# Kernel optimization log

Hardware: AMD Instinct MI355X
Metric: run time of the kernel (lower is better)

Reference implementation:

```python
import jax, jax.numpy as jnp
import numpy as np

LAMBDA = 1.5
B, N = 32, 2048


def setup_inputs() -> dict:
    key = jax.random.key(0)
    ks = jax.random.split(key, 8)
    return {
        "Y_r": jax.random.normal(ks[0], (B, N, N), jnp.float32),
        "Y_i": jax.random.normal(ks[1], (B, N, N), jnp.float32),
        "x_r": jax.random.normal(ks[2], (B, N, 1), jnp.float32),
        "x_i": jax.random.normal(ks[3], (B, N, 1), jnp.float32),
        "x_prev_r": jax.random.normal(ks[4], (B, N, 1), jnp.float32),
        "x_prev_i": jax.random.normal(ks[5], (B, N, 1), jnp.float32),
        "d3_w": jnp.ones((1, 1), jnp.float32),          # Dense(1), ones init
        "d3_b": jnp.zeros((1,), jnp.float32),
        "w1": jax.random.normal(ks[6], (1, 256), jnp.float32) * 0.1,
        "b1": jnp.zeros((256,), jnp.float32),
        "w2": jax.random.normal(ks[7], (256, 1), jnp.float32) * 0.1,
        "b2": jnp.zeros((1,), jnp.float32),
    }


def reference(Y_r, Y_i, x_r, x_i, x_prev_r, x_prev_i, d3_w, d3_b, w1, b1, w2, b2):
    L = LAMBDA
    # complex batched matvec: (B,N,N) @ (B,N,1) -> (B,N,1)
    x1_r = L * (jnp.matmul(Y_r, x_r) - jnp.matmul(Y_i, x_i))
    x1_i = L * (jnp.matmul(Y_r, x_i) + jnp.matmul(Y_i, x_r))
    # Dense(1) on trailing dim of size 1
    x1_r = x1_r @ d3_w + d3_b
    x1_i = x1_i @ d3_w + d3_b
    # |x|^2, mean over N (axis=1), keepdims -> (B,1,1)
    x_abs2_mean = jnp.mean(x_r ** 2 + x_i ** 2, axis=1, keepdims=True)
    scale = -(L ** 2) * (1.0 - x_abs2_mean)
    x1_r = x1_r + scale * x_prev_r
    x1_i = x1_i + scale * x_prev_i
    x1_abs = jnp.sqrt(x1_r ** 2 + x1_i ** 2)
    denom = jnp.maximum(x1_abs, 1e-12)
    # tiny MLP: Dense(256)+relu -> Dense(1) -> tanh
    h = jax.nn.relu(x1_abs @ w1 + b1)
    g = jnp.tanh(h @ w2 + b2)
    q = g / denom
    return (x1_r * q, x1_i * q)
```

## Files before the change

kernel.cpp:

```cpp
#include <hip/hip_runtime.h>
#include <math.h>

#define B_ 32
#define N_ 2048
#define ROWS_PER_BLOCK 16
#define BLOCKS_PER_BATCH (N_ / ROWS_PER_BLOCK)

__global__ __launch_bounds__(256) void scale_kernel(const float* __restrict__ x_r,
                                                    const float* __restrict__ x_i,
                                                    float* __restrict__ scale) {
    const int b = blockIdx.x;
    const int t = threadIdx.x;
    const float* xr = x_r + (size_t)b * N_;
    const float* xi = x_i + (size_t)b * N_;
    float s = 0.f;
    for (int i = t; i < N_; i += 256) {
        float a = xr[i], c = xi[i];
        s += a * a + c * c;
    }
    #pragma unroll
    for (int m = 1; m < 64; m <<= 1) s += __shfl_xor(s, m, 64);
    __shared__ float parts[4];
    if ((t & 63) == 0) parts[t >> 6] = s;
    __syncthreads();
    if (t == 0) {
        float tot = parts[0] + parts[1] + parts[2] + parts[3];
        scale[b] = -2.25f * (1.0f - tot / (float)N_);
    }
}

__global__ __launch_bounds__(256) void sync_block_kernel(
    const float* __restrict__ Yr, const float* __restrict__ Yi,
    const float* __restrict__ x_r, const float* __restrict__ x_i,
    const float* __restrict__ xp_r, const float* __restrict__ xp_i,
    const float* __restrict__ d3w, const float* __restrict__ d3b,
    const float* __restrict__ w1, const float* __restrict__ b1,
    const float* __restrict__ w2, const float* __restrict__ b2,
    const float* __restrict__ scale, float* __restrict__ out)
{
    __shared__ float4 xs_r[N_ / 4];
    __shared__ float4 xs_i[N_ / 4];

    const int t    = threadIdx.x;
    const int lane = t & 63;
    const int wave = t >> 6;
    const int b    = blockIdx.x / BLOCKS_PER_BATCH;
    const int row0 = (blockIdx.x % BLOCKS_PER_BATCH) * ROWS_PER_BLOCK;

    const float4* gxr = (const float4*)(x_r + (size_t)b * N_);
    const float4* gxi = (const float4*)(x_i + (size_t)b * N_);
    for (int i = t; i < N_ / 4; i += 256) {
        xs_r[i] = gxr[i];
        xs_i[i] = gxi[i];
    }
    __syncthreads();

    float w1v[4], b1v[4], w2v[4];
    #pragma unroll
    for (int k = 0; k < 4; ++k) {
        w1v[k] = w1[lane + 64 * k];
        b1v[k] = b1[lane + 64 * k];
        w2v[k] = w2[lane + 64 * k];
    }
    const float d3w_v = d3w[0], d3b_v = d3b[0], b2v = b2[0];
    const float sc = scale[b];

    #pragma unroll
    for (int r = 0; r < 4; ++r) {
        const int row = row0 + wave * 4 + r;
        const float4* yr4 = (const float4*)(Yr + ((size_t)b * N_ + row) * (size_t)N_);
        const float4* yi4 = (const float4*)(Yi + ((size_t)b * N_ + row) * (size_t)N_);

        float rr = 0.f, ri = 0.f, ir = 0.f, ii = 0.f;
        #pragma unroll
        for (int it = 0; it < 8; ++it) {
            const int idx = lane + it * 64;
            float4 a = yr4[idx];
            float4 c = yi4[idx];
            float4 u = xs_r[idx];
            float4 v = xs_i[idx];
            rr += a.x * u.x + a.y * u.y + a.z * u.z + a.w * u.w;
            ri += a.x * v.x + a.y * v.y + a.z * v.z + a.w * v.w;
            ir += c.x * u.x + c.y * u.y + c.z * u.z + c.w * u.w;
            ii += c.x * v.x + c.y * v.y + c.z * v.z + c.w * v.w;
        }
        #pragma unroll
        for (int m = 1; m < 64; m <<= 1) {
            rr += __shfl_xor(rr, m, 64);
            ri += __shfl_xor(ri, m, 64);
            ir += __shfl_xor(ir, m, 64);
            ii += __shfl_xor(ii, m, 64);
        }

        float x1r = 1.5f * (rr - ii);
        float x1i = 1.5f * (ri + ir);
        x1r = x1r * d3w_v + d3b_v;
        x1i = x1i * d3w_v + d3b_v;
        x1r += sc * xp_r[(size_t)b * N_ + row];
        x1i += sc * xp_i[(size_t)b * N_ + row];

        const float xabs  = sqrtf(x1r * x1r + x1i * x1i);
        const float denom = fmaxf(xabs, 1e-12f);

        float p = 0.f;
        #pragma unroll
        for (int k = 0; k < 4; ++k) {
            float h = fmaxf(xabs * w1v[k] + b1v[k], 0.f);
            p += h * w2v[k];
        }
        #pragma unroll
        for (int m = 1; m < 64; m <<= 1) p += __shfl_xor(p, m, 64);

        const float g = tanhf(p + b2v);
        const float q = g / denom;

        if (lane == 0) {
            out[(size_t)b * N_ + row]                    = x1r * q;
            out[(size_t)B_ * N_ + (size_t)b * N_ + row]  = x1i * q;
        }
    }
}

extern "C" void kernel_launch(void* const* d_in, const int* in_sizes, int n_in,
                              void* d_out, int out_size, void* d_ws, size_t ws_size,
                              hipStream_t stream) {
    const float* Yr   = (const float*)d_in[0];
    const float* Yi   = (const float*)d_in[1];
    const float* x_r  = (const float*)d_in[2];
    const float* x_i  = (const float*)d_in[3];
    const float* xp_r = (const float*)d_in[4];
    const float* xp_i = (const float*)d_in[5];
    const float* d3w  = (const float*)d_in[6];
    const float* d3b  = (const float*)d_in[7];
    const float* w1   = (const float*)d_in[8];
    const float* b1   = (const float*)d_in[9];
    const float* w2   = (const float*)d_in[10];
    const float* b2   = (const float*)d_in[11];
    float* out   = (float*)d_out;
    float* scale = (float*)d_ws;

    scale_kernel<<<B_, 256, 0, stream>>>(x_r, x_i, scale);
    sync_block_kernel<<<(B_ * N_) / ROWS_PER_BLOCK, 256, 0, stream>>>(
        Yr, Yi, x_r, x_i, xp_r, xp_i, d3w, d3b, w1, b1, w2, b2, scale, out);
}
```

Measured before the change: 977.1 us.

## Fuse scale reduction into matvec kernel and keep x in registers

```diff
diff --git a/kernel.cpp b/kernel.cpp
--- a/kernel.cpp
+++ b/kernel.cpp
@@ -3,57 +3,35 @@
 
 #define B_ 32
 #define N_ 2048
-#define ROWS_PER_BLOCK 16
+#define ROWS_PER_WAVE 4
+#define WAVES_PER_BLOCK 4
+#define ROWS_PER_BLOCK (ROWS_PER_WAVE * WAVES_PER_BLOCK)
 #define BLOCKS_PER_BATCH (N_ / ROWS_PER_BLOCK)
 
-__global__ __launch_bounds__(256) void scale_kernel(const float* __restrict__ x_r,
-                                                    const float* __restrict__ x_i,
-                                                    float* __restrict__ scale) {
-    const int b = blockIdx.x;
-    const int t = threadIdx.x;
-    const float* xr = x_r + (size_t)b * N_;
-    const float* xi = x_i + (size_t)b * N_;
-    float s = 0.f;
-    for (int i = t; i < N_; i += 256) {
-        float a = xr[i], c = xi[i];
-        s += a * a + c * c;
-    }
-    #pragma unroll
-    for (int m = 1; m < 64; m <<= 1) s += __shfl_xor(s, m, 64);
-    __shared__ float parts[4];
-    if ((t & 63) == 0) parts[t >> 6] = s;
-    __syncthreads();
-    if (t == 0) {
-        float tot = parts[0] + parts[1] + parts[2] + parts[3];
-        scale[b] = -2.25f * (1.0f - tot / (float)N_);
-    }
-}
-
-__global__ __launch_bounds__(256) void sync_block_kernel(
+__global__ __launch_bounds__(256) void fused_sync_kernel(
     const float* __restrict__ Yr, const float* __restrict__ Yi,
     const float* __restrict__ x_r, const float* __restrict__ x_i,
     const float* __restrict__ xp_r, const float* __restrict__ xp_i,
     const float* __restrict__ d3w, const float* __restrict__ d3b,
     const float* __restrict__ w1, const float* __restrict__ b1,
     const float* __restrict__ w2, const float* __restrict__ b2,
-    const float* __restrict__ scale, float* __restrict__ out)
+    float* __restrict__ out)
 {
-    __shared__ float4 xs_r[N_ / 4];
-    __shared__ float4 xs_i[N_ / 4];
-
     const int t    = threadIdx.x;
     const int lane = t & 63;
     const int wave = t >> 6;
     const int b    = blockIdx.x / BLOCKS_PER_BATCH;
-    const int row0 = (blockIdx.x % BLOCKS_PER_BATCH) * ROWS_PER_BLOCK;
+    const int row0 = (blockIdx.x % BLOCKS_PER_BATCH) * ROWS_PER_BLOCK
+                   + wave * ROWS_PER_WAVE;
 
     const float4* gxr = (const float4*)(x_r + (size_t)b * N_);
     const float4* gxi = (const float4*)(x_i + (size_t)b * N_);
-    for (int i = t; i < N_ / 4; i += 256) {
-        xs_r[i] = gxr[i];
-        xs_i[i] = gxi[i];
+    float4 xr[8], xi[8];
+    #pragma unroll
+    for (int it = 0; it < 8; ++it) {
+        xr[it] = gxr[lane + it * 64];
+        xi[it] = gxi[lane + it * 64];
     }
-    __syncthreads();
 
     float w1v[4], b1v[4], w2v[4];
     #pragma unroll
@@ -63,60 +41,85 @@
         w2v[k] = w2[lane + 64 * k];
     }
     const float d3w_v = d3w[0], d3b_v = d3b[0], b2v = b2[0];
-    const float sc = scale[b];
+
+    float ss = 0.f;
+    #pragma unroll
+    for (int it = 0; it < 8; ++it) {
+        ss += xr[it].x * xr[it].x + xr[it].y * xr[it].y
+            + xr[it].z * xr[it].z + xr[it].w * xr[it].w;
+        ss += xi[it].x * xi[it].x + xi[it].y * xi[it].y
+            + xi[it].z * xi[it].z + xi[it].w * xi[it].w;
+    }
+    #pragma unroll
+    for (int m = 1; m < 64; m <<= 1) ss += __shfl_xor(ss, m, 64);
+    const float sc = -2.25f * (1.0f - ss * (1.0f / (float)N_));
+
+    const size_t ybase = ((size_t)b * N_ + row0) * (size_t)N_;
+    float sr[4] = {0.f, 0.f, 0.f, 0.f};
+    float si[4] = {0.f, 0.f, 0.f, 0.f};
 
     #pragma unroll
+    for (int it = 0; it < 8; ++it) {
+        const int idx = lane + it * 64;
+        float4 a[4], c[4];
+        #pragma unroll
+        for (int r = 0; r < 4; ++r) {
+            a[r] = *(const float4*)(Yr + ybase + (size_t)r * N_ + 4 * (size_t)idx);
+            c[r] = *(const float4*)(Yi + ybase + (size_t)r * N_ + 4 * (size_t)idx);
+        }
+        const float4 u = xr[it];
+        const float4 v = xi[it];
+        #pragma unroll
+        for (int r = 0; r < 4; ++r) {
+            sr[r] += a[r].x * u.x + a[r].y * u.y + a[r].z * u.z + a[r].w * u.w
+                   - (c[r].x * v.x + c[r].y * v.y + c[r].z * v.z + c[r].w * v.w);
+            si[r] += a[r].x * v.x + a[r].y * v.y + a[r].z * v.z + a[r].w * v.w
+                   + c[r].x * u.x + c[r].y * u.y + c[r].z * u.z + c[r].w * u.w;
+        }
+    }
+
+    #pragma unroll
+    for (int m = 1; m < 64; m <<= 1) {
+        #pragma unroll
+        for (int r = 0; r < 4; ++r) {
+            sr[r] += __shfl_xor(sr[r], m, 64);
+            si[r] += __shfl_xor(si[r], m, 64);
+        }
+    }
+
+    float x1r[4], x1i[4], xabs[4], p[4];
+    #pragma unroll
     for (int r = 0; r < 4; ++r) {
-        const int row = row0 + wave * 4 + r;
-        const float4* yr4 = (const float4*)(Yr + ((size_t)b * N_ + row) * (size_t)N_);
-        const float4* yi4 = (const float4*)(Yi + ((size_t)b * N_ + row) * (size_t)N_);
-
-        float rr = 0.f, ri = 0.f, ir = 0.f, ii = 0.f;
-        #pragma unroll
-        for (int it = 0; it < 8; ++it) {
-            const int idx = lane + it * 64;
-            float4 a = yr4[idx];
-            float4 c = yi4[idx];
-            float4 u = xs_r[idx];
-            float4 v = xs_i[idx];
-            rr += a.x * u.x + a.y * u.y + a.z * u.z + a.w * u.w;
-            ri += a.x * v.x + a.y * v.y + a.z * v.z + a.w * v.w;
-            ir += c.x * u.x + c.y * u.y + c.z * u.z + c.w * u.w;
-            ii += c.x * v.x + c.y * v.y + c.z * v.z + c.w * v.w;
-        }
-        #pragma unroll
-        for (int m = 1; m < 64; m <<= 1) {
-            rr += __shfl_xor(rr, m, 64);
-            ri += __shfl_xor(ri, m, 64);
-            ir += __shfl_xor(ir, m, 64);
-            ii += __shfl_xor(ii, m, 64);
-        }
-
-        float x1r = 1.5f * (rr - ii);
-        float x1i = 1.5f * (ri + ir);
-        x1r = x1r * d3w_v + d3b_v;
-        x1i = x1i * d3w_v + d3b_v;
-        x1r += sc * xp_r[(size_t)b * N_ + row];
-        x1i += sc * xp_i[(size_t)b * N_ + row];
-
-        const float xabs  = sqrtf(x1r * x1r + x1i * x1i);
-        const float denom = fmaxf(xabs, 1e-12f);
-
-        float p = 0.f;
+        float vr = 1.5f * sr[r];
+        float vi = 1.5f * si[r];
+        vr = vr * d3w_v + d3b_v;
+        vi = vi * d3w_v + d3b_v;
+        vr += sc * xp_r[(size_t)b * N_ + row0 + r];
+        vi += sc * xp_i[(size_t)b * N_ + row0 + r];
+        x1r[r] = vr;
+        x1i[r] = vi;
+        xabs[r] = sqrtf(vr * vr + vi * vi);
+        float pp = 0.f;
         #pragma unroll
         for (int k = 0; k < 4; ++k) {
-            float h = fmaxf(xabs * w1v[k] + b1v[k], 0.f);
-            p += h * w2v[k];
+            float h = fmaxf(xabs[r] * w1v[k] + b1v[k], 0.f);
+            pp += h * w2v[k];
         }
+        p[r] = pp;
+    }
+    #pragma unroll
+    for (int m = 1; m < 64; m <<= 1) {
         #pragma unroll
-        for (int m = 1; m < 64; m <<= 1) p += __shfl_xor(p, m, 64);
+        for (int r = 0; r < 4; ++r) p[r] += __shfl_xor(p[r], m, 64);
+    }
 
-        const float g = tanhf(p + b2v);
-        const float q = g / denom;
-
-        if (lane == 0) {
-            out[(size_t)b * N_ + row]                    = x1r * q;
-            out[(size_t)B_ * N_ + (size_t)b * N_ + row]  = x1i * q;
+    if (lane == 0) {
+        #pragma unroll
+        for (int r = 0; r < 4; ++r) {
+            const float g = tanhf(p[r] + b2v);
+            const float q = g / fmaxf(xabs[r], 1e-12f);
+            out[(size_t)b * N_ + row0 + r]                    = x1r[r] * q;
+            out[(size_t)B_ * N_ + (size_t)b * N_ + row0 + r]  = x1i[r] * q;
         }
     }
 }
@@ -136,10 +139,8 @@
     const float* b1   = (const float*)d_in[9];
     const float* w2   = (const float*)d_in[10];
     const float* b2   = (const float*)d_in[11];
-    float* out   = (float*)d_out;
-    float* scale = (float*)d_ws;
+    float* out = (float*)d_out;
 
-    scale_kernel<<<B_, 256, 0, stream>>>(x_r, x_i, scale);
-    sync_block_kernel<<<(B_ * N_) / ROWS_PER_BLOCK, 256, 0, stream>>>(
-        Yr, Yi, x_r, x_i, xp_r, xp_i, d3w, d3b, w1, b1, w2, b2, scale, out);
+    fused_sync_kernel<<<(B_ * N_) / ROWS_PER_BLOCK, 256, 0, stream>>>(
+        Yr, Yi, x_r, x_i, xp_r, xp_i, d3w, d3b, w1, b1, w2, b2, out);
 }
```

New measurement: 975.0 us. About the same (-0.2%).
